# Kernel optimization log

Measured on AMD Instinct MI355X. Metric: run time of the kernel, lower is better.

The kernel has to match this reference:

```python
import jax, jax.numpy as jnp
import numpy as np

N, E = 50000, 400000
HID, HT = 128, 128
HEADS, C = 4, 128  # TransformerConv heads=4, out_channels=hidden_X


def setup_inputs() -> dict:
    key = jax.random.key(0)
    ks = jax.random.split(key, 16)
    s = lambda k, shape, fan: jax.random.normal(k, shape, jnp.float32) / np.sqrt(fan)
    return {
        "edge_index": jax.random.randint(ks[0], (2, E), 0, N, dtype=jnp.int32),
        "h_X": jax.random.normal(ks[1], (N, HID), jnp.float32),
        "h_t": jax.random.normal(ks[2], (1, HT), jnp.float32),
        # TransformerConv params: lin_query/key/value: (HID -> HEADS*C), lin_skip: (HID -> C)
        "Wq": s(ks[3], (HID, HEADS * C), HID), "bq": jnp.zeros((HEADS * C,), jnp.float32),
        "Wk": s(ks[4], (HID, HEADS * C), HID), "bk": jnp.zeros((HEADS * C,), jnp.float32),
        "Wv": s(ks[5], (HID, HEADS * C), HID), "bv": jnp.zeros((HEADS * C,), jnp.float32),
        "Wskip": s(ks[6], (HID, C), HID), "bskip": jnp.zeros((C,), jnp.float32),
        # update_X: Linear(HID+HT -> HID), LayerNorm(HID)
        "Wup": s(ks[7], (HID + HT, HID), HID + HT), "bup": jnp.zeros((HID,), jnp.float32),
        "gamma": jnp.ones((HID,), jnp.float32), "beta": jnp.zeros((HID,), jnp.float32),
    }


def transformer_conv(h_X, edge_index, Wq, bq, Wk, bk, Wv, bv, Wskip, bskip):
    n = h_X.shape[0]
    src, dst = edge_index[0], edge_index[1]  # messages flow src -> dst
    q = (h_X @ Wq + bq).reshape(n, HEADS, C)
    k = (h_X @ Wk + bk).reshape(n, HEADS, C)
    v = (h_X @ Wv + bv).reshape(n, HEADS, C)
    # per-edge attention scores [E, H]
    score = jnp.einsum('ehc,ehc->eh', q[dst], k[src]) / np.sqrt(C)
    # segment softmax over incoming edges of each destination node
    m = jax.ops.segment_max(score, dst, num_segments=n)          # [N, H]
    ex = jnp.exp(score - m[dst])                                 # [E, H]
    denom = jax.ops.segment_sum(ex, dst, num_segments=n)        # [N, H]
    alpha = ex / denom[dst]                                      # [E, H]
    agg = jax.ops.segment_sum(alpha[..., None] * v[src], dst, num_segments=n)  # [N, H, C]
    out = agg.mean(axis=1)                                       # concat=False -> mean over heads
    return out + h_X @ Wskip + bskip                             # root_weight=True


def reference(edge_index, h_X, h_t, Wq, bq, Wk, bk, Wv, bv, Wskip, bskip,
              Wup, bup, gamma, beta):
    n = h_X.shape[0]
    h_att = transformer_conv(h_X, edge_index, Wq, bq, Wk, bk, Wv, bv, Wskip, bskip)
    h_t_exp = jnp.broadcast_to(h_t, (n, h_t.shape[1]))
    h = jnp.concatenate([h_att, h_t_exp], axis=1)
    h = jax.nn.relu(h @ Wup + bup)
    # LayerNorm (eps=1e-5); Dropout is identity in eval
    mu = h.mean(axis=-1, keepdims=True)
    var = ((h - mu) ** 2).mean(axis=-1, keepdims=True)
    return (h - mu) / jnp.sqrt(var + 1e-5) * gamma + beta
```

## Files before the change

### kernel.cpp

```cpp
#include <hip/hip_runtime.h>

typedef unsigned short u16;
typedef unsigned int   u32;

#define HID   128
#define HEADS 4
#define CH    128
#define HC    512
#define KVW   1024
#define UT    64

typedef __bf16 bf16x8v __attribute__((ext_vector_type(8)));
typedef float  f32x4v  __attribute__((ext_vector_type(4)));
union FragU { uint4 u; bf16x8v b; };

static __device__ __forceinline__ float bf2f(u16 u) {
  union { u32 u; float f; } x;
  x.u = ((u32)u) << 16;
  return x.f;
}
static __device__ __forceinline__ u16 f2bf(float f) {
  union { float f; u32 u; } x;
  x.f = f;
  u32 r = x.u + 0x7fffu + ((x.u >> 16) & 1u);
  return (u16)(r >> 16);
}

static __device__ __forceinline__ void unpack8(uint4 raw, float* dst) {
  dst[0] = bf2f((u16)(raw.x & 0xffffu));
  dst[1] = bf2f((u16)(raw.x >> 16));
  dst[2] = bf2f((u16)(raw.y & 0xffffu));
  dst[3] = bf2f((u16)(raw.y >> 16));
  dst[4] = bf2f((u16)(raw.z & 0xffffu));
  dst[5] = bf2f((u16)(raw.z >> 16));
  dst[6] = bf2f((u16)(raw.w & 0xffffu));
  dst[7] = bf2f((u16)(raw.w >> 16));
}

__global__ void pre_kernel(const float* __restrict__ hX,
                           u16* __restrict__ hpack, int N, int totH,
                           const float* __restrict__ Wq,
                           const float* __restrict__ Wk,
                           const float* __restrict__ Wv,
                           const float* __restrict__ Wsk,
                           u16* __restrict__ Wp,
                           const float* __restrict__ h_t,
                           const float* __restrict__ Wup,
                           const float* __restrict__ bup,
                           float* __restrict__ cvec,
                           const int* __restrict__ dst_idx,
                           int* __restrict__ deg, int E, int HBLK, int WBLK) {
  int b = blockIdx.x;
  int t = threadIdx.x;
  if (b < HBLK) {
    int i = b * 256 + t;
    if (i >= totH) return;
    int j = i & 7;
    int lane = (i >> 3) & 63;
    int kc = (i >> 9) & 3;
    int ntile = i >> 11;
    int node = ntile * 16 + (lane & 15);
    int k = kc * 32 + (lane >> 4) * 8 + j;
    float v = (node < N) ? hX[(size_t)node * HID + k] : 0.f;
    hpack[i] = f2bf(v);
  } else if (b < HBLK + WBLK) {
    int i = (b - HBLK) * 256 + t;
    if (i >= 128 * 1664) return;
    int j = i & 7;
    int lane = (i >> 3) & 63;
    int kc = (i >> 9) & 3;
    int ct = i >> 11;
    int n = ct * 16 + (lane & 15);
    int k = kc * 32 + (lane >> 4) * 8 + j;
    float w;
    if (n < 512) w = Wq[(size_t)k * HC + n];
    else if (n < 1024) w = Wk[(size_t)k * HC + (n - 512)];
    else if (n < 1536) w = Wv[(size_t)k * HC + (n - 1024)];
    else w = Wsk[(size_t)k * HID + (n - 1536)];
    Wp[i] = f2bf(w);
  } else if (b == HBLK + WBLK) {
    if (t < 128) {
      float acc = bup[t];
      for (int k = 0; k < 128; ++k)
        acc = fmaf(h_t[k], Wup[(size_t)(128 + k) * 128 + t], acc);
      cvec[t] = acc;
    }
  } else {
    int e = (b - HBLK - WBLK - 1) * 256 + t;
    if (e < E) atomicAdd(&deg[dst_idx[e]], 1);
  }
}

__global__ void blocksum_kernel(const int* deg, int* bsums, int n) {
  __shared__ int buf[256];
  int i = blockIdx.x * 256 + threadIdx.x;
  int v = 0;
  if (i < n) v = deg[i];
  buf[threadIdx.x] = v;
  __syncthreads();
  for (int off = 128; off > 0; off >>= 1) {
    if (threadIdx.x < off) buf[threadIdx.x] += buf[threadIdx.x + off];
    __syncthreads();
  }
  if (threadIdx.x == 0) bsums[blockIdx.x] = buf[0];
}

__global__ void scanb_kernel(const int* bsums, int* boffs, int nb) {
  __shared__ int buf[256];
  __shared__ int carry_s;
  int tid = threadIdx.x;
  if (tid == 0) carry_s = 0;
  __syncthreads();
  for (int base = 0; base < nb; base += 256) {
    int i = base + tid;
    int v = 0;
    if (i < nb) v = bsums[i];
    buf[tid] = v;
    __syncthreads();
    for (int off = 1; off < 256; off <<= 1) {
      int t = 0;
      if (tid >= off) t = buf[tid - off];
      __syncthreads();
      buf[tid] += t;
      __syncthreads();
    }
    int incl = buf[tid] + carry_s;
    if (i < nb) boffs[i] = incl - v;
    __syncthreads();
    if (tid == 255) carry_s = incl;
    __syncthreads();
  }
}

__global__ void scanfinal_kernel(const int* deg, const int* boffs,
                                 int* row_ptr, int* cursor, int n) {
  __shared__ int buf[256];
  int tid = threadIdx.x;
  int i = blockIdx.x * 256 + tid;
  int v = 0;
  if (i < n) v = deg[i];
  buf[tid] = v;
  __syncthreads();
  for (int off = 1; off < 256; off <<= 1) {
    int t = 0;
    if (tid >= off) t = buf[tid - off];
    __syncthreads();
    buf[tid] += t;
    __syncthreads();
  }
  int incl = buf[tid] + boffs[blockIdx.x];
  if (i < n) {
    row_ptr[i + 1] = incl;
    cursor[i] = incl - v;
  }
  if (i == 0) row_ptr[0] = 0;
}

__global__ void scatter_kernel(const int* src_idx, const int* dst_idx,
                               int* cursor, int* col, int E) {
  int e = blockIdx.x * 256 + threadIdx.x;
  if (e < E) {
    int pos = atomicAdd(&cursor[dst_idx[e]], 1);
    col[pos] = src_idx[e];
  }
}

__global__ __launch_bounds__(256) void mfma_proj_kernel(
    const u16* __restrict__ hpack, const u16* __restrict__ Wp,
    const float* __restrict__ bq, const float* __restrict__ bk,
    const float* __restrict__ bv, const float* __restrict__ bsk,
    u16* __restrict__ qb, u16* __restrict__ kvb,
    float* __restrict__ skipf, int N) {
  int t = threadIdx.x;
  int wv = t >> 6;
  int L = t & 63;
  int bx = blockIdx.x;
  int my0 = blockIdx.y * 8;

  FragU Bf[2][4];
  const u16* wb0 = Wp + (size_t)(bx * 8 + wv * 2) * 2048;
#pragma unroll
  for (int cc = 0; cc < 2; ++cc)
#pragma unroll
    for (int kc = 0; kc < 4; ++kc)
      Bf[cc][kc].u = *(const uint4*)(wb0 + cc * 2048 + kc * 512 + L * 8);

  int colq = L & 15;
  int quad = L >> 4;
  u16* outB_[2];
  int stride_[2];
  float bval[2];
  int nl_[2];
  int isF32_[2];
#pragma unroll
  for (int cc = 0; cc < 2; ++cc) {
    int n = (bx * 8 + wv * 2 + cc) * 16 + colq;
    const float* bias;
    if (n < 512) {
      outB_[cc] = qb; bias = bq; nl_[cc] = n; stride_[cc] = HC; isF32_[cc] = 0;
    } else if (n < 1024) {
      outB_[cc] = kvb; bias = bk; nl_[cc] = n - 512; stride_[cc] = KVW;
      isF32_[cc] = 0;
    } else if (n < 1536) {
      outB_[cc] = kvb; bias = bv; nl_[cc] = n - 512; stride_[cc] = KVW;
      isF32_[cc] = 0;
    } else {
      outB_[cc] = (u16*)skipf; bias = bsk; nl_[cc] = n - 1536; stride_[cc] = 0;
      isF32_[cc] = 1;
    }
    bval[cc] = bias[nl_[cc]];
  }

  const u16* ha = hpack + (size_t)my0 * 2048;

  for (int mt = 0; mt < 8; mt += 2) {
    FragU a0[4], a1[4];
#pragma unroll
    for (int kc = 0; kc < 4; ++kc) {
      a0[kc].u = *(const uint4*)(ha + (size_t)mt * 2048 + kc * 512 + L * 8);
      a1[kc].u =
          *(const uint4*)(ha + (size_t)(mt + 1) * 2048 + kc * 512 + L * 8);
    }

    f32x4v ac00 = (f32x4v){0.f, 0.f, 0.f, 0.f};
    f32x4v ac01 = (f32x4v){0.f, 0.f, 0.f, 0.f};
    f32x4v ac10 = (f32x4v){0.f, 0.f, 0.f, 0.f};
    f32x4v ac11 = (f32x4v){0.f, 0.f, 0.f, 0.f};
#pragma unroll
    for (int kc = 0; kc < 4; ++kc) {
      ac00 = __builtin_amdgcn_mfma_f32_16x16x32_bf16(a0[kc].b, Bf[0][kc].b,
                                                     ac00, 0, 0, 0);
      ac01 = __builtin_amdgcn_mfma_f32_16x16x32_bf16(a0[kc].b, Bf[1][kc].b,
                                                     ac01, 0, 0, 0);
      ac10 = __builtin_amdgcn_mfma_f32_16x16x32_bf16(a1[kc].b, Bf[0][kc].b,
                                                     ac10, 0, 0, 0);
      ac11 = __builtin_amdgcn_mfma_f32_16x16x32_bf16(a1[kc].b, Bf[1][kc].b,
                                                     ac11, 0, 0, 0);
    }

#pragma unroll
    for (int half = 0; half < 2; ++half) {
      int nodeBase = (my0 + mt + half) * 16 + quad * 4;
#pragma unroll
      for (int cc = 0; cc < 2; ++cc) {
        const f32x4v& a =
            half ? (cc ? ac11 : ac10) : (cc ? ac01 : ac00);
        if (isF32_[cc]) {
#pragma unroll
          for (int rg = 0; rg < 4; ++rg) {
            int node = nodeBase + rg;
            if (node < N)
              skipf[(size_t)node * HID + nl_[cc]] = a[rg] + bval[cc];
          }
        } else {
          u16* ob = outB_[cc];
          int st = stride_[cc];
#pragma unroll
          for (int rg = 0; rg < 4; ++rg) {
            int node = nodeBase + rg;
            if (node < N)
              ob[(size_t)node * st + nl_[cc]] = f2bf(a[rg] + bval[cc]);
          }
        }
      }
    }
  }
}

__global__ void fused_attn_kernel(const u16* __restrict__ qb,
                                  const u16* __restrict__ kvb,
                                  const int* __restrict__ row_ptr,
                                  const int* __restrict__ col_src,
                                  float* out, int N) {
  int node = blockIdx.x * 4 + (threadIdx.x >> 6);
  if (node >= N) return;
  int lane = threadIdx.x & 63;
  int head = lane >> 4;
  int r = lane & 15;
  int foff = head * CH + r * 8;
  const float sscale = 0.08838834764831845f;

  float qf[8];
  unpack8(*(const uint4*)(qb + (size_t)node * HC + foff), qf);

  float m = -3.402823466e38f;
  float l = 0.f;
  float acc[8];
  for (int j = 0; j < 8; ++j) acc[j] = 0.f;

  int e0 = row_ptr[node];
  int e1 = row_ptr[node + 1];
  int e = e0;

  for (; e + 4 <= e1; e += 4) {
    int s0 = col_src[e];
    int s1 = col_src[e + 1];
    int s2 = col_src[e + 2];
    int s3 = col_src[e + 3];
    const u16* r0p = kvb + (size_t)s0 * KVW + foff;
    const u16* r1p = kvb + (size_t)s1 * KVW + foff;
    const u16* r2p = kvb + (size_t)s2 * KVW + foff;
    const u16* r3p = kvb + (size_t)s3 * KVW + foff;
    uint4 k0 = *(const uint4*)(r0p);
    uint4 k1 = *(const uint4*)(r1p);
    uint4 k2 = *(const uint4*)(r2p);
    uint4 k3 = *(const uint4*)(r3p);
    uint4 v0 = *(const uint4*)(r0p + 512);
    uint4 v1 = *(const uint4*)(r1p + 512);
    uint4 v2 = *(const uint4*)(r2p + 512);
    uint4 v3 = *(const uint4*)(r3p + 512);

    float kf0[8], kf1[8], kf2[8], kf3[8];
    unpack8(k0, kf0);
    unpack8(k1, kf1);
    unpack8(k2, kf2);
    unpack8(k3, kf3);
    float p0 = 0.f, p1 = 0.f, p2 = 0.f, p3 = 0.f;
    for (int j = 0; j < 8; ++j) {
      p0 = fmaf(kf0[j], qf[j], p0);
      p1 = fmaf(kf1[j], qf[j], p1);
      p2 = fmaf(kf2[j], qf[j], p2);
      p3 = fmaf(kf3[j], qf[j], p3);
    }
    p0 += __shfl_xor(p0, 1);
    p1 += __shfl_xor(p1, 1);
    p2 += __shfl_xor(p2, 1);
    p3 += __shfl_xor(p3, 1);
    p0 += __shfl_xor(p0, 2);
    p1 += __shfl_xor(p1, 2);
    p2 += __shfl_xor(p2, 2);
    p3 += __shfl_xor(p3, 2);
    p0 += __shfl_xor(p0, 4);
    p1 += __shfl_xor(p1, 4);
    p2 += __shfl_xor(p2, 4);
    p3 += __shfl_xor(p3, 4);
    p0 += __shfl_xor(p0, 8);
    p1 += __shfl_xor(p1, 8);
    p2 += __shfl_xor(p2, 8);
    p3 += __shfl_xor(p3, 8);
    float sc0 = p0 * sscale;
    float sc1 = p1 * sscale;
    float sc2 = p2 * sscale;
    float sc3 = p3 * sscale;
    float mnew = fmaxf(fmaxf(m, fmaxf(sc0, sc1)), fmaxf(sc2, sc3));
    float so = __expf(m - mnew);
    float pe0 = __expf(sc0 - mnew);
    float pe1 = __expf(sc1 - mnew);
    float pe2 = __expf(sc2 - mnew);
    float pe3 = __expf(sc3 - mnew);
    l = l * so + (pe0 + pe1) + (pe2 + pe3);
    float vf0[8], vf1[8], vf2[8], vf3[8];
    unpack8(v0, vf0);
    unpack8(v1, vf1);
    unpack8(v2, vf2);
    unpack8(v3, vf3);
    for (int j = 0; j < 8; ++j) {
      float add = fmaf(pe0, vf0[j],
                       fmaf(pe1, vf1[j], fmaf(pe2, vf2[j], pe3 * vf3[j])));
      acc[j] = fmaf(acc[j], so, add);
    }
    m = mnew;
  }

  for (; e < e1; ++e) {
    int s0 = col_src[e];
    const u16* r0p = kvb + (size_t)s0 * KVW + foff;
    uint4 k0 = *(const uint4*)(r0p);
    uint4 v0 = *(const uint4*)(r0p + 512);
    float kf0[8];
    unpack8(k0, kf0);
    float p0 = 0.f;
    for (int j = 0; j < 8; ++j) p0 = fmaf(kf0[j], qf[j], p0);
    p0 += __shfl_xor(p0, 1);
    p0 += __shfl_xor(p0, 2);
    p0 += __shfl_xor(p0, 4);
    p0 += __shfl_xor(p0, 8);
    float sc0 = p0 * sscale;
    float mnew = fmaxf(m, sc0);
    float so = __expf(m - mnew);
    float pe0 = __expf(sc0 - mnew);
    l = l * so + pe0;
    float vf0[8];
    unpack8(v0, vf0);
    for (int j = 0; j < 8; ++j) acc[j] = fmaf(acc[j], so, pe0 * vf0[j]);
    m = mnew;
  }

  float inv = 0.f;
  if (l > 0.f) inv = 1.0f / l;
  float val[8];
  for (int j = 0; j < 8; ++j) {
    float x = acc[j] * inv;
    x += __shfl_xor(x, 16);
    x += __shfl_xor(x, 32);
    val[j] = x * 0.25f;
  }

  if (head == 0) {
    float* p = out + (size_t)node * HID + r * 8;
    float4 a = *(const float4*)(p);
    float4 b = *(const float4*)(p + 4);
    a.x += val[0]; a.y += val[1]; a.z += val[2]; a.w += val[3];
    b.x += val[4]; b.y += val[5]; b.z += val[6]; b.w += val[7];
    *(float4*)(p) = a;
    *(float4*)(p + 4) = b;
  }
}

__global__ __launch_bounds__(512) void ATTLayer_19396072308956_kernel(
    float* out, const float* __restrict__ Wup, const float* __restrict__ cvec,
    const float* __restrict__ gamma, const float* __restrict__ beta, int N) {
  __shared__ float Wl[64 * 128];
  __shared__ float Hl[UT * 128];
  int t = threadIdx.x;
  int n0 = blockIdx.x * UT;

  for (int i = t * 4; i < UT * 128; i += 2048) {
    int node = n0 + (i >> 7);
    float4 v;
    if (node < N) {
      v = *(const float4*)(out + (size_t)node * HID + (i & 127));
    } else {
      v.x = 0.f; v.y = 0.f; v.z = 0.f; v.w = 0.f;
    }
    *(float4*)(Hl + i) = v;
  }

  int wv = t >> 6;
  int r = t & 63;
  int c0 = 2 * r;
  float2 cv = *(const float2*)(cvec + c0);
  float a0[8];
  float a1[8];
  for (int j = 0; j < 8; ++j) {
    a0[j] = cv.x;
    a1[j] = cv.y;
  }

  for (int ph = 0; ph < 2; ++ph) {
    __syncthreads();
    for (int i = t * 4; i < 64 * 128; i += 2048) {
      *(float4*)(Wl + i) = *(const float4*)(Wup + (size_t)ph * 64 * 128 + i);
    }
    __syncthreads();
    const float* hbase = Hl + (wv * 8) * 128 + ph * 64;
#pragma unroll 8
    for (int k = 0; k < 64; ++k) {
      float2 w2 = *(const float2*)(Wl + k * 128 + c0);
      for (int j = 0; j < 8; ++j) {
        float h = hbase[j * 128 + k];
        a0[j] = fmaf(h, w2.x, a0[j]);
        a1[j] = fmaf(h, w2.y, a1[j]);
      }
    }
  }

  float2 g = *(const float2*)(gamma + c0);
  float2 b = *(const float2*)(beta + c0);
  for (int j = 0; j < 8; ++j) {
    int node = n0 + wv * 8 + j;
    float r0 = fmaxf(a0[j], 0.f);
    float r1 = fmaxf(a1[j], 0.f);
    float s = r0 + r1;
    for (int msk = 1; msk < 64; msk <<= 1) s += __shfl_xor(s, msk);
    float mean = s * (1.0f / 128.0f);
    float d0 = r0 - mean;
    float d1 = r1 - mean;
    float sq = d0 * d0 + d1 * d1;
    for (int msk = 1; msk < 64; msk <<= 1) sq += __shfl_xor(sq, msk);
    float rstd = rsqrtf(sq * (1.0f / 128.0f) + 1e-5f);
    if (node < N) {
      float2 o;
      o.x = d0 * rstd * g.x + b.x;
      o.y = d1 * rstd * g.y + b.y;
      *(float2*)(out + (size_t)node * HID + c0) = o;
    }
  }
}

extern "C" void kernel_launch(void* const* d_in, const int* in_sizes, int n_in,
                              void* d_out, int out_size, void* d_ws,
                              size_t ws_size, hipStream_t stream) {
  (void)n_in;
  (void)out_size;
  (void)ws_size;

  const int* edge_index = (const int*)d_in[0];
  const float* hX    = (const float*)d_in[1];
  const float* h_t   = (const float*)d_in[2];
  const float* Wq    = (const float*)d_in[3];
  const float* bq    = (const float*)d_in[4];
  const float* Wk    = (const float*)d_in[5];
  const float* bk    = (const float*)d_in[6];
  const float* Wv    = (const float*)d_in[7];
  const float* bv    = (const float*)d_in[8];
  const float* Wskip = (const float*)d_in[9];
  const float* bskip = (const float*)d_in[10];
  const float* Wup   = (const float*)d_in[11];
  const float* bup   = (const float*)d_in[12];
  const float* gamma = (const float*)d_in[13];
  const float* beta  = (const float*)d_in[14];

  const int E = in_sizes[0] / 2;
  const int N = in_sizes[1] / HID;
  const int* src_idx = edge_index;
  const int* dst_idx = edge_index + E;
  const int NB = (N + 255) / 256;
  const int NTILES = (N + 15) / 16;
  const int NTILES8 = ((NTILES + 7) / 8) * 8;

  char* w = (char*)d_ws;
  size_t off = 0;
  float* cvec = (float*)(w + off);
  off += 256 * 4;
  int* deg = (int*)(w + off);
  off += ((size_t)N * 4 + 255) / 256 * 256;
  int* row_ptr = (int*)(w + off);
  off += ((size_t)(N + 1) * 4 + 255) / 256 * 256;
  int* cursor = (int*)(w + off);
  off += ((size_t)N * 4 + 255) / 256 * 256;
  int* bsums = (int*)(w + off);
  off += ((size_t)NB * 4 + 255) / 256 * 256;
  int* boffs = (int*)(w + off);
  off += ((size_t)NB * 4 + 255) / 256 * 256;
  int* col = (int*)(w + off);
  off += ((size_t)E * 4 + 255) / 256 * 256;
  u16* hpack = (u16*)(w + off);
  off += ((size_t)NTILES8 * 2048 * 2 + 255) / 256 * 256;
  u16* Wp = (u16*)(w + off);
  off += ((size_t)128 * 1664 * 2 + 255) / 256 * 256;
  u16* bigA = (u16*)(w + off);
  off += ((size_t)N * HC * 2 + 255) / 256 * 256;
  u16* bigKV = (u16*)(w + off);
  off += ((size_t)N * KVW * 2 + 255) / 256 * 256;

  float* out = (float*)d_out;

  hipMemsetAsync(deg, 0, (size_t)N * 4, stream);
  int totH = NTILES8 * 2048;
  int HBLK = (totH + 255) / 256;
  int WBLK = (128 * 1664 + 255) / 256;
  int EBLK = (E + 255) / 256;
  pre_kernel<<<HBLK + WBLK + 1 + EBLK, 256, 0, stream>>>(
      hX, hpack, N, totH, Wq, Wk, Wv, Wskip, Wp, h_t, Wup, bup, cvec, dst_idx,
      deg, E, HBLK, WBLK);

  blocksum_kernel<<<NB, 256, 0, stream>>>(deg, bsums, N);
  scanb_kernel<<<1, 256, 0, stream>>>(bsums, boffs, NB);
  scanfinal_kernel<<<NB, 256, 0, stream>>>(deg, boffs, row_ptr, cursor, N);
  scatter_kernel<<<EBLK, 256, 0, stream>>>(src_idx, dst_idx, cursor, col, E);

  mfma_proj_kernel<<<dim3(13, NTILES8 / 8), 256, 0, stream>>>(
      hpack, Wp, bq, bk, bv, bskip, bigA, bigKV, out, N);

  fused_attn_kernel<<<(N + 3) / 4, 256, 0, stream>>>(bigA, bigKV, row_ptr,
                                                     col, out, N);

  ATTLayer_19396072308956_kernel<<<(N + UT - 1) / UT, 512, 0, stream>>>(
      out, Wup, cvec, gamma, beta, N);
}
```

Before: 390.7 us.

## Fuse edge scatter into projection launch and remap update kernel thread layout

The CSR scatter kernel is folded into the MFMA projection kernel as extra leading blocks, which removes one launch and lets the scatter run alongside the projection blocks. The final Linear+LayerNorm kernel is restructured so 16 lanes share one node with 8 output columns each. Its tile shrinks to 32 nodes with a padded shared-memory row stride, and the LayerNorm reductions now need only 4 shuffle steps. The trade-off is that the update kernel re-stages Wup for every 32 nodes instead of every 64, doubling weight reload traffic.

After: 390.8 us. Within noise of the previous version (+0.0%).

```diff
diff --git a/kernel.cpp b/kernel.cpp
--- a/kernel.cpp
+++ b/kernel.cpp
@@ -8,7 +8,7 @@
 #define CH    128
 #define HC    512
 #define KVW   1024
-#define UT    64
+#define UTN   32
 
 typedef __bf16 bf16x8v __attribute__((ext_vector_type(8)));
 typedef float  f32x4v  __attribute__((ext_vector_type(4)));
@@ -156,26 +156,29 @@
   if (i == 0) row_ptr[0] = 0;
 }
 
-__global__ void scatter_kernel(const int* src_idx, const int* dst_idx,
-                               int* cursor, int* col, int E) {
-  int e = blockIdx.x * 256 + threadIdx.x;
-  if (e < E) {
-    int pos = atomicAdd(&cursor[dst_idx[e]], 1);
-    col[pos] = src_idx[e];
-  }
-}
-
 __global__ __launch_bounds__(256) void mfma_proj_kernel(
     const u16* __restrict__ hpack, const u16* __restrict__ Wp,
     const float* __restrict__ bq, const float* __restrict__ bk,
     const float* __restrict__ bv, const float* __restrict__ bsk,
     u16* __restrict__ qb, u16* __restrict__ kvb,
-    float* __restrict__ skipf, int N) {
+    float* __restrict__ skipf, int N,
+    const int* __restrict__ src_idx, const int* __restrict__ dst_idx,
+    int* __restrict__ cursor, int* __restrict__ col, int E, int EBLK) {
+  int bid = blockIdx.x;
+  if (bid < EBLK) {
+    int e = bid * 256 + threadIdx.x;
+    if (e < E) {
+      int pos = atomicAdd(&cursor[dst_idx[e]], 1);
+      col[pos] = src_idx[e];
+    }
+    return;
+  }
+  int pbid = bid - EBLK;
   int t = threadIdx.x;
   int wv = t >> 6;
   int L = t & 63;
-  int bx = blockIdx.x;
-  int my0 = blockIdx.y * 8;
+  int bx = pbid % 13;
+  int my0 = (pbid / 13) * 8;
 
   FragU Bf[2][4];
   const u16* wb0 = Wp + (size_t)(bx * 8 + wv * 2) * 2048;
@@ -411,31 +414,35 @@
     float* out, const float* __restrict__ Wup, const float* __restrict__ cvec,
     const float* __restrict__ gamma, const float* __restrict__ beta, int N) {
   __shared__ float Wl[64 * 128];
-  __shared__ float Hl[UT * 128];
+  __shared__ float Hl[UTN * 132];
   int t = threadIdx.x;
-  int n0 = blockIdx.x * UT;
-
-  for (int i = t * 4; i < UT * 128; i += 2048) {
-    int node = n0 + (i >> 7);
+  int n0 = blockIdx.x * UTN;
+
+  for (int i = t * 4; i < UTN * 128; i += 2048) {
+    int row = i >> 7;
+    int cc = i & 127;
+    int node = n0 + row;
     float4 v;
     if (node < N) {
-      v = *(const float4*)(out + (size_t)node * HID + (i & 127));
+      v = *(const float4*)(out + (size_t)node * HID + cc);
     } else {
       v.x = 0.f; v.y = 0.f; v.z = 0.f; v.w = 0.f;
     }
-    *(float4*)(Hl + i) = v;
+    *(float4*)(Hl + row * 132 + cc) = v;
   }
 
   int wv = t >> 6;
-  int r = t & 63;
-  int c0 = 2 * r;
-  float2 cv = *(const float2*)(cvec + c0);
-  float a0[8];
-  float a1[8];
-  for (int j = 0; j < 8; ++j) {
-    a0[j] = cv.x;
-    a1[j] = cv.y;
-  }
+  int lane = t & 63;
+  int nsub = lane >> 4;
+  int cg = lane & 15;
+  int nloc = wv * 4 + nsub;
+  int node = n0 + nloc;
+  int c0 = cg * 8;
+
+  float4 ca = *(const float4*)(cvec + c0);
+  float4 cb = *(const float4*)(cvec + c0 + 4);
+  float a0 = ca.x, a1 = ca.y, a2 = ca.z, a3 = ca.w;
+  float a4 = cb.x, a5 = cb.y, a6 = cb.z, a7 = cb.w;
 
   for (int ph = 0; ph < 2; ++ph) {
     __syncthreads();
@@ -443,38 +450,58 @@
       *(float4*)(Wl + i) = *(const float4*)(Wup + (size_t)ph * 64 * 128 + i);
     }
     __syncthreads();
-    const float* hbase = Hl + (wv * 8) * 128 + ph * 64;
+    const float* hrow = Hl + nloc * 132 + ph * 64;
 #pragma unroll 8
     for (int k = 0; k < 64; ++k) {
-      float2 w2 = *(const float2*)(Wl + k * 128 + c0);
-      for (int j = 0; j < 8; ++j) {
-        float h = hbase[j * 128 + k];
-        a0[j] = fmaf(h, w2.x, a0[j]);
-        a1[j] = fmaf(h, w2.y, a1[j]);
-      }
-    }
-  }
-
-  float2 g = *(const float2*)(gamma + c0);
-  float2 b = *(const float2*)(beta + c0);
-  for (int j = 0; j < 8; ++j) {
-    int node = n0 + wv * 8 + j;
-    float r0 = fmaxf(a0[j], 0.f);
-    float r1 = fmaxf(a1[j], 0.f);
-    float s = r0 + r1;
-    for (int msk = 1; msk < 64; msk <<= 1) s += __shfl_xor(s, msk);
-    float mean = s * (1.0f / 128.0f);
-    float d0 = r0 - mean;
-    float d1 = r1 - mean;
-    float sq = d0 * d0 + d1 * d1;
-    for (int msk = 1; msk < 64; msk <<= 1) sq += __shfl_xor(sq, msk);
-    float rstd = rsqrtf(sq * (1.0f / 128.0f) + 1e-5f);
-    if (node < N) {
-      float2 o;
-      o.x = d0 * rstd * g.x + b.x;
-      o.y = d1 * rstd * g.y + b.y;
-      *(float2*)(out + (size_t)node * HID + c0) = o;
-    }
+      float hk = hrow[k];
+      float4 wa = *(const float4*)(Wl + k * 128 + c0);
+      float4 wb = *(const float4*)(Wl + k * 128 + c0 + 4);
+      a0 = fmaf(hk, wa.x, a0);
+      a1 = fmaf(hk, wa.y, a1);
+      a2 = fmaf(hk, wa.z, a2);
+      a3 = fmaf(hk, wa.w, a3);
+      a4 = fmaf(hk, wb.x, a4);
+      a5 = fmaf(hk, wb.y, a5);
+      a6 = fmaf(hk, wb.z, a6);
+      a7 = fmaf(hk, wb.w, a7);
+    }
+  }
+
+  float r0 = fmaxf(a0, 0.f), r1 = fmaxf(a1, 0.f);
+  float r2 = fmaxf(a2, 0.f), r3 = fmaxf(a3, 0.f);
+  float r4 = fmaxf(a4, 0.f), r5 = fmaxf(a5, 0.f);
+  float r6 = fmaxf(a6, 0.f), r7 = fmaxf(a7, 0.f);
+  float s = ((r0 + r1) + (r2 + r3)) + ((r4 + r5) + (r6 + r7));
+  s += __shfl_xor(s, 1);
+  s += __shfl_xor(s, 2);
+  s += __shfl_xor(s, 4);
+  s += __shfl_xor(s, 8);
+  float mean = s * (1.0f / 128.0f);
+  float d0 = r0 - mean, d1 = r1 - mean, d2 = r2 - mean, d3 = r3 - mean;
+  float d4 = r4 - mean, d5 = r5 - mean, d6 = r6 - mean, d7 = r7 - mean;
+  float sq = ((d0 * d0 + d1 * d1) + (d2 * d2 + d3 * d3)) +
+             ((d4 * d4 + d5 * d5) + (d6 * d6 + d7 * d7));
+  sq += __shfl_xor(sq, 1);
+  sq += __shfl_xor(sq, 2);
+  sq += __shfl_xor(sq, 4);
+  sq += __shfl_xor(sq, 8);
+  float rstd = rsqrtf(sq * (1.0f / 128.0f) + 1e-5f);
+  if (node < N) {
+    float4 ga = *(const float4*)(gamma + c0);
+    float4 gb = *(const float4*)(gamma + c0 + 4);
+    float4 ba = *(const float4*)(beta + c0);
+    float4 bb = *(const float4*)(beta + c0 + 4);
+    float4 o1, o2;
+    o1.x = d0 * rstd * ga.x + ba.x;
+    o1.y = d1 * rstd * ga.y + ba.y;
+    o1.z = d2 * rstd * ga.z + ba.z;
+    o1.w = d3 * rstd * ga.w + ba.w;
+    o2.x = d4 * rstd * gb.x + bb.x;
+    o2.y = d5 * rstd * gb.y + bb.y;
+    o2.z = d6 * rstd * gb.z + bb.z;
+    o2.w = d7 * rstd * gb.w + bb.w;
+    *(float4*)(out + (size_t)node * HID + c0) = o1;
+    *(float4*)(out + (size_t)node * HID + c0 + 4) = o2;
   }
 }
 
@@ -548,14 +575,15 @@
   blocksum_kernel<<<NB, 256, 0, stream>>>(deg, bsums, N);
   scanb_kernel<<<1, 256, 0, stream>>>(bsums, boffs, NB);
   scanfinal_kernel<<<NB, 256, 0, stream>>>(deg, boffs, row_ptr, cursor, N);
-  scatter_kernel<<<EBLK, 256, 0, stream>>>(src_idx, dst_idx, cursor, col, E);
-
-  mfma_proj_kernel<<<dim3(13, NTILES8 / 8), 256, 0, stream>>>(
-      hpack, Wp, bq, bk, bv, bskip, bigA, bigKV, out, N);
+
+  int PROJ_BLOCKS = 13 * (NTILES8 / 8);
+  mfma_proj_kernel<<<EBLK + PROJ_BLOCKS, 256, 0, stream>>>(
+      hpack, Wp, bq, bk, bv, bskip, bigA, bigKV, out, N, src_idx, dst_idx,
+      cursor, col, E, EBLK);
 
   fused_attn_kernel<<<(N + 3) / 4, 256, 0, stream>>>(bigA, bigKV, row_ptr,
                                                      col, out, N);
 
-  ATTLayer_19396072308956_kernel<<<(N + UT - 1) / UT, 512, 0, stream>>>(
+  ATTLayer_19396072308956_kernel<<<(N + UTN - 1) / UTN, 512, 0, stream>>>(
       out, Wup, cvec, gamma, beta, N);
 }
```
